# Kernel tuning notes

Hardware: AMD Instinct MI355X
Metric: run time of the kernel (lower is better)

Reference implementation:

```python
import jax, jax.numpy as jnp
import numpy as np

BN_EPS = 1e-5


def setup_inputs() -> dict:
    key = jax.random.key(0)
    ks = jax.random.split(key, 10)
    B, C, L = 16, 512, 1024
    scale = 1.0 / np.sqrt(C)
    inp = {
        "x": jax.random.normal(ks[0], (B, C, L), dtype=jnp.float32),
        "gamma": jnp.ones((C,), jnp.float32),
        "beta": jnp.zeros((C,), jnp.float32),
        "Wq": jax.random.normal(ks[1], (C, C), jnp.float32) * scale,
        "bq": jnp.zeros((C,), jnp.float32),
        "Wk": jax.random.normal(ks[2], (C, C), jnp.float32) * scale,
        "bk": jnp.zeros((C,), jnp.float32),
        "Wv": jax.random.normal(ks[3], (C, C), jnp.float32) * scale,
        "bv": jnp.zeros((C,), jnp.float32),
        "Wp": jax.random.normal(ks[4], (C, C), jnp.float32) * scale,
        "bp": jnp.zeros((C,), jnp.float32),
    }
    return inp


def _pointwise(W, b, h):
    # Conv1d with kernel_size=1 == per-position linear: [C_out,C_in] x [B,C_in,L]
    return jnp.einsum("oc,bcl->bol", W, h) + b[None, :, None]


def reference(x, gamma, beta, Wq, bq, Wk, bk, Wv, bv, Wp, bp):
    B, C, L = x.shape
    # BatchNorm1d (training-mode batch statistics over batch & length dims)
    mean = jnp.mean(x, axis=(0, 2), keepdims=True)
    var = jnp.var(x, axis=(0, 2), keepdims=True)
    hn = (x - mean) * jax.lax.rsqrt(var + BN_EPS)
    hn = hn * gamma[None, :, None] + beta[None, :, None]

    q = _pointwise(Wq, bq, hn)  # [B,C,L]
    k = _pointwise(Wk, bk, hn)
    v = _pointwise(Wv, bv, hn)

    # attn[b,i,j] = sum_c q[b,c,i] k[b,c,j] / sqrt(C); i=query pos, j=key pos
    attn = jnp.einsum("bci,bcj->bij", q, k) * (C ** -0.5)
    attn = jax.nn.softmax(attn, axis=-1)

    # out[b,c,i] = sum_j attn[b,i,j] v[b,c,j]
    h_ = jnp.einsum("bij,bcj->bci", attn, v)
    h_ = _pointwise(Wp, bp, h_)
    return x + h_
```

## Files before the change

### kernel.cpp

```cpp
#include <hip/hip_runtime.h>
#include <hip/hip_bf16.h>


#define BB 16
#define CC 512
#define LL 1024

typedef __bf16 bf16x8 __attribute__((ext_vector_type(8)));
typedef float  f32x4  __attribute__((ext_vector_type(4)));

__device__ inline unsigned short bf16_bits(float f) {
  __hip_bfloat16 h = __float2bfloat16(f);
  return __builtin_bit_cast(unsigned short, h);
}
__device__ inline float bits_lo(unsigned int u) {
  return __builtin_bit_cast(float, u << 16);
}
__device__ inline float bits_hi(unsigned int u) {
  return __builtin_bit_cast(float, u & 0xffff0000u);
}

__global__ __launch_bounds__(256) void bn_stats(
    const float* __restrict__ x, const float* __restrict__ gamma,
    const float* __restrict__ beta, float* __restrict__ scl,
    float* __restrict__ sft, float* __restrict__ rowsum) {
  int c = blockIdx.x;
  int t = threadIdx.x;
  int g = c * 256 + t;
  if (g < 16384) rowsum[g] = 0.f;
  float s = 0.f, s2 = 0.f;
  for (int b = 0; b < BB; ++b) {
    float4 v = ((const float4*)(x + ((size_t)(b * CC + c)) * LL))[t];
    s  += v.x + v.y + v.z + v.w;
    s2 += v.x * v.x + v.y * v.y + v.z * v.z + v.w * v.w;
  }
  for (int m = 32; m; m >>= 1) { s += __shfl_xor(s, m, 64); s2 += __shfl_xor(s2, m, 64); }
  __shared__ float rs[4], rs2[4];
  int wave = t >> 6, lane = t & 63;
  if (lane == 0) { rs[wave] = s; rs2[wave] = s2; }
  __syncthreads();
  if (t == 0) {
    float S  = rs[0] + rs[1] + rs[2] + rs[3];
    float S2 = rs2[0] + rs2[1] + rs2[2] + rs2[3];
    float mean = S * (1.f / 16384.f);
    float var  = S2 * (1.f / 16384.f) - mean * mean;
    float sc = gamma[c] * rsqrtf(var + 1e-5f);
    scl[c] = sc;
    sft[c] = beta[c] - mean * sc;
  }
}

__global__ __launch_bounds__(256) void cast4(
    const float* __restrict__ Wq, const float* __restrict__ Wk,
    const float* __restrict__ Wv, const float* __restrict__ Wp,
    __hip_bfloat16* __restrict__ Wqkv, __hip_bfloat16* __restrict__ Wpb) {
  int m = blockIdx.y;
  const float* src = m == 0 ? Wq : m == 1 ? Wk : m == 2 ? Wv : Wp;
  __hip_bfloat16* dst = m < 3 ? Wqkv + (size_t)m * 262144 : Wpb;
  int i = blockIdx.x * 256 + threadIdx.x;
  float4 v = ((const float4*)src)[i];
  ushort4 o;
  o.x = bf16_bits(v.x); o.y = bf16_bits(v.y);
  o.z = bf16_bits(v.z); o.w = bf16_bits(v.w);
  ((ushort4*)dst)[i] = o;
}

__global__ __launch_bounds__(256) void norm_t(
    const float* __restrict__ x, const float* __restrict__ scl,
    const float* __restrict__ sft, __hip_bfloat16* __restrict__ hnT) {
  __shared__ float tile[32][33];
  int l0 = blockIdx.x * 32, c0 = blockIdx.y * 32, b = blockIdx.z;
  int t = threadIdx.x;
#pragma unroll
  for (int i = 0; i < 4; ++i) {
    int idx = t + i * 256;
    int cc = idx >> 5, ll = idx & 31;
    tile[cc][ll] = x[((size_t)(b * CC + c0 + cc)) * LL + l0 + ll];
  }
  __syncthreads();
#pragma unroll
  for (int i = 0; i < 2; ++i) {
    int idx = t + i * 256;
    int ll = idx >> 4, cc = (idx & 15) * 2;
    float v0 = tile[cc][ll] * scl[c0 + cc] + sft[c0 + cc];
    float v1 = tile[cc + 1][ll] * scl[c0 + cc + 1] + sft[c0 + cc + 1];
    ushort2 o; o.x = bf16_bits(v0); o.y = bf16_bits(v1);
    *(ushort2*)(hnT + ((size_t)(b * LL + l0 + ll)) * CC + c0 + cc) = o;
  }
}

__device__ __forceinline__ void gemm_core(
    const __hip_bfloat16* __restrict__ A, int lda,
    const __hip_bfloat16* __restrict__ B, int ldb, int K,
    __hip_bfloat16* sA, __hip_bfloat16* sB, f32x4 (&acc)[4][4]) {
  const int tid = threadIdx.x;
  const int wave = tid >> 6, lane = tid & 63;
  const int wm = (wave >> 1) * 64, wn = (wave & 1) * 64;
  const int row0 = tid >> 2;
  const int ke0 = (((tid & 3) ^ ((tid >> 3) & 3)) * 8);
  const int fr = lane & 15;
  const int q = lane >> 4;
  const int colA = ((q ^ ((fr >> 1) & 3)) * 8);
  for (int k0 = 0; k0 < K; k0 += 32) {
    __syncthreads();
#pragma unroll
    for (int it = 0; it < 2; ++it) {
      const __hip_bfloat16* ga = A + (size_t)(it * 64 + row0) * lda + (k0 + ke0);
      const __hip_bfloat16* gb = B + (size_t)(it * 64 + row0) * ldb + (k0 + ke0);
      __builtin_amdgcn_global_load_lds(
          (__attribute__((address_space(1))) void*)(void*)ga,
          (__attribute__((address_space(3))) void*)(sA + (it * 256 + wave * 64) * 8),
          16, 0, 0);
      __builtin_amdgcn_global_load_lds(
          (__attribute__((address_space(1))) void*)(void*)gb,
          (__attribute__((address_space(3))) void*)(sB + (it * 256 + wave * 64) * 8),
          16, 0, 0);
    }
    __syncthreads();
    bf16x8 af[4], bfr[4];
#pragma unroll
    for (int i = 0; i < 4; ++i) {
      af[i]  = *(const bf16x8*)(sA + (wm + i * 16 + fr) * 32 + colA);
      bfr[i] = *(const bf16x8*)(sB + (wn + i * 16 + fr) * 32 + colA);
    }
#pragma unroll
    for (int i = 0; i < 4; ++i)
#pragma unroll
      for (int j = 0; j < 4; ++j)
        acc[i][j] = __builtin_amdgcn_mfma_f32_16x16x32_bf16(af[i], bfr[j], acc[i][j], 0, 0, 0);
  }
}

__device__ __forceinline__ void gemm_core8p(
    const __hip_bfloat16* __restrict__ A, int lda,
    const __hip_bfloat16* __restrict__ B, int ldb, int K,
    __hip_bfloat16* sA, __hip_bfloat16* sB, f32x4 (&acc)[8][4]) {
  const int tid = threadIdx.x;
  const int wave = tid >> 6, lane = tid & 63;
  const int fr = lane & 15, q = lane >> 4;
  const int wm = (wave >> 2) * 128, wn = (wave & 3) * 64;
  const int srow = tid >> 3;
  const int sko = ((tid & 7) ^ (srow & 7)) * 8;
  const int NT = K >> 6;
  const int ck0 = (q ^ (fr & 7)) * 8;

#define STG_A(tt, u)                                                           \
  __builtin_amdgcn_global_load_lds(                                            \
      (__attribute__((address_space(1))) void*)(void*)(                        \
          A + (size_t)((u) * 64 + srow) * lda + (tt) * 64 + sko),              \
      (__attribute__((address_space(3))) void*)(                               \
          sA + ((tt) & 1) * 16384 + (u) * 4096 + wave * 512), 16, 0, 0)
#define STG_B(tt, u)                                                           \
  __builtin_amdgcn_global_load_lds(                                            \
      (__attribute__((address_space(1))) void*)(void*)(                        \
          B + (size_t)((u) * 64 + srow) * ldb + (tt) * 64 + sko),              \
      (__attribute__((address_space(3))) void*)(                               \
          sB + ((tt) & 1) * 16384 + (u) * 4096 + wave * 512), 16, 0, 0)

  STG_A(0, 0); STG_A(0, 1); STG_A(0, 2); STG_A(0, 3);
  STG_B(0, 0); STG_B(0, 1); STG_B(0, 2); STG_B(0, 3);
  STG_A(1, 0); STG_A(1, 1); STG_A(1, 2); STG_A(1, 3);
  STG_B(1, 0); STG_B(1, 1); STG_B(1, 2); STG_B(1, 3);

  for (int t = 0; t < NT; ++t) {
    const __hip_bfloat16* pA = sA + (t & 1) * 16384;
    const __hip_bfloat16* pB = sB + (t & 1) * 16384;
    const int rowA = wm + fr, rowB = wn + fr;
    const bool st = (t + 2) < NT;
    bf16x8 a03[4][2], a47[4][2], b01[2][2], b23[2][2];

    __builtin_amdgcn_sched_barrier(0);
    if (t == NT - 1) { asm volatile("s_waitcnt vmcnt(0)" ::: "memory"); }
    else             { asm volatile("s_waitcnt vmcnt(8)" ::: "memory"); }
    __builtin_amdgcn_s_barrier();
    __builtin_amdgcn_sched_barrier(0);

#pragma unroll
    for (int i = 0; i < 4; ++i) {
      a03[i][0] = *(const bf16x8*)(pA + (rowA + i * 16) * 64 + ck0);
      a03[i][1] = *(const bf16x8*)(pA + (rowA + i * 16) * 64 + (ck0 ^ 32));
    }
#pragma unroll
    for (int j = 0; j < 2; ++j) {
      b01[j][0] = *(const bf16x8*)(pB + (rowB + j * 16) * 64 + ck0);
      b01[j][1] = *(const bf16x8*)(pB + (rowB + j * 16) * 64 + (ck0 ^ 32));
    }
    __builtin_amdgcn_s_barrier();
    asm volatile("s_waitcnt lgkmcnt(0)" ::: "memory");
    __builtin_amdgcn_sched_barrier(0);
    __builtin_amdgcn_s_setprio(1);
#pragma unroll
    for (int i = 0; i < 4; ++i)
#pragma unroll
      for (int j = 0; j < 2; ++j) {
        acc[i][j] = __builtin_amdgcn_mfma_f32_16x16x32_bf16(a03[i][0], b01[j][0], acc[i][j], 0, 0, 0);
        acc[i][j] = __builtin_amdgcn_mfma_f32_16x16x32_bf16(a03[i][1], b01[j][1], acc[i][j], 0, 0, 0);
      }
    __builtin_amdgcn_s_setprio(0);
    __builtin_amdgcn_s_barrier();
    __builtin_amdgcn_sched_barrier(0);

#pragma unroll
    for (int j = 0; j < 2; ++j) {
      b23[j][0] = *(const bf16x8*)(pB + (rowB + 32 + j * 16) * 64 + ck0);
      b23[j][1] = *(const bf16x8*)(pB + (rowB + 32 + j * 16) * 64 + (ck0 ^ 32));
    }
    if (st) { STG_A(t + 2, 0); STG_A(t + 2, 2); }
    __builtin_amdgcn_s_barrier();
    asm volatile("s_waitcnt lgkmcnt(0)" ::: "memory");
    __builtin_amdgcn_sched_barrier(0);
    __builtin_amdgcn_s_setprio(1);
#pragma unroll
    for (int i = 0; i < 4; ++i)
#pragma unroll
      for (int j = 0; j < 2; ++j) {
        acc[i][2 + j] = __builtin_amdgcn_mfma_f32_16x16x32_bf16(a03[i][0], b23[j][0], acc[i][2 + j], 0, 0, 0);
        acc[i][2 + j] = __builtin_amdgcn_mfma_f32_16x16x32_bf16(a03[i][1], b23[j][1], acc[i][2 + j], 0, 0, 0);
      }
    __builtin_amdgcn_s_setprio(0);
    __builtin_amdgcn_s_barrier();
    __builtin_amdgcn_sched_barrier(0);

#pragma unroll
    for (int i = 0; i < 4; ++i) {
      a47[i][0] = *(const bf16x8*)(pA + (rowA + 64 + i * 16) * 64 + ck0);
      a47[i][1] = *(const bf16x8*)(pA + (rowA + 64 + i * 16) * 64 + (ck0 ^ 32));
    }
    if (st) { STG_B(t + 2, 0); STG_B(t + 2, 1); STG_B(t + 2, 2); }
    __builtin_amdgcn_s_barrier();
    asm volatile("s_waitcnt lgkmcnt(0)" ::: "memory");
    __builtin_amdgcn_sched_barrier(0);
    __builtin_amdgcn_s_setprio(1);
#pragma unroll
    for (int i = 0; i < 4; ++i)
#pragma unroll
      for (int j = 0; j < 2; ++j) {
        acc[4 + i][j] = __builtin_amdgcn_mfma_f32_16x16x32_bf16(a47[i][0], b01[j][0], acc[4 + i][j], 0, 0, 0);
        acc[4 + i][j] = __builtin_amdgcn_mfma_f32_16x16x32_bf16(a47[i][1], b01[j][1], acc[4 + i][j], 0, 0, 0);
      }
    __builtin_amdgcn_s_setprio(0);
    __builtin_amdgcn_s_barrier();
    __builtin_amdgcn_sched_barrier(0);

    if (st) { STG_B(t + 2, 3); STG_A(t + 2, 1); STG_A(t + 2, 3); }
    __builtin_amdgcn_s_barrier();
    __builtin_amdgcn_sched_barrier(0);
    __builtin_amdgcn_s_setprio(1);
#pragma unroll
    for (int i = 0; i < 4; ++i)
#pragma unroll
      for (int j = 0; j < 2; ++j) {
        acc[4 + i][2 + j] = __builtin_amdgcn_mfma_f32_16x16x32_bf16(a47[i][0], b23[j][0], acc[4 + i][2 + j], 0, 0, 0);
        acc[4 + i][2 + j] = __builtin_amdgcn_mfma_f32_16x16x32_bf16(a47[i][1], b23[j][1], acc[4 + i][2 + j], 0, 0, 0);
      }
    __builtin_amdgcn_s_setprio(0);
  }
#undef STG_A
#undef STG_B
}

__global__ __launch_bounds__(512, 2) void gemm_qkv256(
    const __hip_bfloat16* __restrict__ Wb, const __hip_bfloat16* __restrict__ hnT,
    __hip_bfloat16* __restrict__ qT, __hip_bfloat16* __restrict__ kT,
    __hip_bfloat16* __restrict__ vN,
    const float* __restrict__ bq, const float* __restrict__ bk,
    const float* __restrict__ bv) {
  __shared__ __align__(16) __hip_bfloat16 smem[4 * 16384];
  __hip_bfloat16* sA = smem;
  __hip_bfloat16* sB = smem + 32768;
  const int m0 = blockIdx.y * 256, n0 = blockIdx.x * 256;
  f32x4 acc[8][4] = {};
  gemm_core8p(Wb + (size_t)m0 * 512, 512, hnT + (size_t)n0 * 512, 512, 512,
              sA, sB, acc);
  const int tid = threadIdx.x;
  const int lane = tid & 63, wave = tid >> 6;
  const int wm = (wave >> 2) * 128, wn = (wave & 3) * 64;
  const int crow = (lane >> 4) * 4, ccol = lane & 15;
  const int id = m0 >> 9;
  const int mloc0 = (m0 & 511) + wm;
  const float* bias = id == 0 ? bq : id == 1 ? bk : bv;
  if (id < 2) {
    __hip_bfloat16* D = id == 0 ? qT : kT;
    const int mc0 = m0 & 511;
    __syncthreads();
#pragma unroll
    for (int h = 0; h < 2; ++h) {
      if ((wn >> 7) == h) {
        const int wnL = wn & 127;
#pragma unroll
        for (int i = 0; i < 8; ++i) {
          int mg = mloc0 + i * 16 + crow;
          int mr = wm + i * 16 + crow;
          float bv4[4];
#pragma unroll
          for (int r = 0; r < 4; ++r) bv4[r] = bias[mg + r];
#pragma unroll
          for (int j = 0; j < 4; ++j) {
            int colL = wnL + j * 16 + ccol;
            ushort4 o;
            o.x = bf16_bits(acc[i][j][0] + bv4[0]);
            o.y = bf16_bits(acc[i][j][1] + bv4[1]);
            o.z = bf16_bits(acc[i][j][2] + bv4[2]);
            o.w = bf16_bits(acc[i][j][3] + bv4[3]);
            *(ushort4*)(smem + colL * 264 + mr) = o;
          }
        }
      }
      __syncthreads();
#pragma unroll
      for (int rep = 0; rep < 8; ++rep) {
        int idx = rep * 512 + tid;
        int col = idx >> 5, c8 = idx & 31;
        bf16x8 v = *(const bf16x8*)(smem + col * 264 + c8 * 8);
        *(bf16x8*)(D + (size_t)(n0 + h * 128 + col) * 512 + mc0 + c8 * 8) = v;
      }
      __syncthreads();
    }
  } else {
#pragma unroll
    for (int i = 0; i < 8; ++i) {
      int mg = mloc0 + i * 16 + crow;
      float bv4[4];
#pragma unroll
      for (int r = 0; r < 4; ++r) bv4[r] = bias[mg + r];
#pragma unroll
      for (int j = 0; j < 4; ++j) {
        int ngf = n0 + wn + j * 16 + ccol;
        int b = ngf >> 10, l = ngf & 1023;
        __hip_bfloat16* D = vN + ((size_t)b * CC + mg) * LL + l;
#pragma unroll
        for (int r = 0; r < 4; ++r)
          D[(size_t)r * LL] = __float2bfloat16(acc[i][j][r] + bv4[r]);
      }
    }
  }
}

__global__ __launch_bounds__(512, 2) void gemm_s256_exp(
    const __hip_bfloat16* __restrict__ qT, const __hip_bfloat16* __restrict__ kT,
    __hip_bfloat16* __restrict__ Sb, float* __restrict__ rowsum) {
  __shared__ __align__(16) __hip_bfloat16 sA[2 * 16384];
  __shared__ __align__(16) __hip_bfloat16 sB[2 * 16384];
  const int bat = blockIdx.z;
  const int m0 = blockIdx.y * 256, n0 = blockIdx.x * 256;
  const size_t sLC = (size_t)LL * CC;
  f32x4 acc[8][4] = {};
  gemm_core8p(qT + (size_t)bat * sLC + (size_t)m0 * 512, 512,
              kT + (size_t)bat * sLC + (size_t)n0 * 512, 512, 512,
              sA, sB, acc);
  const int lane = threadIdx.x & 63, wave = threadIdx.x >> 6;
  const int wm = (wave >> 2) * 128, wn = (wave & 3) * 64;
  const int crow = (lane >> 4) * 4, ccol = lane & 15;
  __hip_bfloat16* D = Sb + (size_t)bat * LL * LL;
  float* rs = rowsum + (size_t)bat * LL;
  const float scale = 0.04419417382415922f;
#pragma unroll
  for (int i = 0; i < 8; ++i) {
    int mg = m0 + wm + i * 16 + crow;
    float sp[4] = {0.f, 0.f, 0.f, 0.f};
#pragma unroll
    for (int j = 0; j < 4; ++j) {
      int ng = n0 + wn + j * 16 + ccol;
#pragma unroll
      for (int r = 0; r < 4; ++r) {
        float e = __expf(acc[i][j][r] * scale);
        sp[r] += e;
        D[(size_t)(mg + r) * LL + ng] = __float2bfloat16(e);
      }
    }
#pragma unroll
    for (int r = 0; r < 4; ++r) {
      for (int m = 8; m; m >>= 1) sp[r] += __shfl_xor(sp[r], m, 64);
    }
    if (ccol == 0) {
#pragma unroll
      for (int r = 0; r < 4; ++r) atomicAdd(&rs[mg + r], sp[r]);
    }
  }
}

template <int MODE, bool BIAS>
__global__ __launch_bounds__(256, 3) void gemm_tn(
    const __hip_bfloat16* __restrict__ A, int lda, size_t strideA,
    const __hip_bfloat16* __restrict__ B, int ldb, size_t strideB,
    void* __restrict__ Dp, int ldd, size_t strideD,
    const float* __restrict__ bias, float scale,
    const float* __restrict__ resid, size_t strideR,
    const float* __restrict__ rowdiv, int K) {
  __shared__ __align__(16) __hip_bfloat16 sA[128 * 32];
  __shared__ __align__(16) __hip_bfloat16 sB[128 * 32];
  const int bat = blockIdx.z;
  const int m0 = blockIdx.y * 128, n0 = blockIdx.x * 128;
  f32x4 acc[4][4] = {};
  gemm_core(A + (size_t)bat * strideA + (size_t)m0 * lda, lda,
            B + (size_t)bat * strideB + (size_t)n0 * ldb, ldb, K, sA, sB, acc);
  const int lane = threadIdx.x & 63, wave = threadIdx.x >> 6;
  const int wm = (wave >> 1) * 64, wn = (wave & 1) * 64;
  const int crow = (lane >> 4) * 4, ccol = lane & 15;
  if constexpr (MODE == 0) {
    __hip_bfloat16* D = (__hip_bfloat16*)Dp + (size_t)bat * strideD;
#pragma unroll
    for (int i = 0; i < 4; ++i) {
      int mg = m0 + wm + i * 16 + crow;
      float bv4[4];
#pragma unroll
      for (int r = 0; r < 4; ++r) bv4[r] = BIAS ? bias[mg + r] : 0.f;
#pragma unroll
      for (int j = 0; j < 4; ++j) {
        int ng = n0 + wn + j * 16 + ccol;
#pragma unroll
        for (int r = 0; r < 4; ++r)
          D[(size_t)(mg + r) * ldd + ng] =
              __float2bfloat16(acc[i][j][r] * scale + bv4[r]);
      }
    }
  } else if constexpr (MODE == 1) {
    __hip_bfloat16* D = (__hip_bfloat16*)Dp + (size_t)bat * strideD;
    const float* rsb = rowdiv + (size_t)bat * LL;
#pragma unroll
    for (int i = 0; i < 4; ++i) {
      int mg = m0 + wm + i * 16 + crow;
      float rinv[4];
#pragma unroll
      for (int r = 0; r < 4; ++r) rinv[r] = 1.f / rsb[mg + r];
#pragma unroll
      for (int j = 0; j < 4; ++j) {
        int ng = n0 + wn + j * 16 + ccol;
#pragma unroll
        for (int r = 0; r < 4; ++r)
          D[(size_t)(mg + r) * ldd + ng] =
              __float2bfloat16(acc[i][j][r] * rinv[r]);
      }
    }
  } else {
    float* D = (float*)Dp + (size_t)bat * strideD;
#pragma unroll
    for (int i = 0; i < 4; ++i) {
      int mg = m0 + wm + i * 16 + crow;
      float bv4[4];
#pragma unroll
      for (int r = 0; r < 4; ++r) bv4[r] = BIAS ? bias[mg + r] : 0.f;
#pragma unroll
      for (int j = 0; j < 4; ++j) {
        int ng = n0 + wn + j * 16 + ccol;
        const float* rsrc = resid + (size_t)bat * strideR + (size_t)mg * ldd + ng;
        float* dst = D + (size_t)mg * ldd + ng;
#pragma unroll
        for (int r = 0; r < 4; ++r)
          dst[(size_t)r * ldd] = acc[i][j][r] * scale + bv4[r] + rsrc[(size_t)r * ldd];
      }
    }
  }
}

extern "C" void kernel_launch(void* const* d_in, const int* in_sizes, int n_in,
                              void* d_out, int out_size, void* d_ws, size_t ws_size,
                              hipStream_t stream) {
  const float* x     = (const float*)d_in[0];
  const float* gamma = (const float*)d_in[1];
  const float* beta  = (const float*)d_in[2];
  const float* Wq    = (const float*)d_in[3];
  const float* bq    = (const float*)d_in[4];
  const float* Wk    = (const float*)d_in[5];
  const float* bk    = (const float*)d_in[6];
  const float* Wv    = (const float*)d_in[7];
  const float* bv    = (const float*)d_in[8];
  const float* Wp    = (const float*)d_in[9];
  const float* bp    = (const float*)d_in[10];
  float* out = (float*)d_out;

  char* ws = (char*)d_ws;
  float* scl = (float*)ws;
  float* sft = scl + 512;
  __hip_bfloat16* Wqkvb = (__hip_bfloat16*)(ws + 4096);
  __hip_bfloat16* Wpb = Wqkvb + 786432;
  __hip_bfloat16* hnT = Wpb + 262144;
  __hip_bfloat16* qT  = hnT + 8388608;
  __hip_bfloat16* kT  = qT + 8388608;
  __hip_bfloat16* vN  = kT + 8388608;
  __hip_bfloat16* Sb  = vN + 8388608;
  float* rowsum = (float*)(Sb + 16777216);
  __hip_bfloat16* HT  = hnT;

  bn_stats<<<512, 256, 0, stream>>>(x, gamma, beta, scl, sft, rowsum);
  cast4<<<dim3(256, 4), 256, 0, stream>>>(Wq, Wk, Wv, Wp, Wqkvb, Wpb);
  norm_t<<<dim3(32, 16, 16), 256, 0, stream>>>(x, scl, sft, hnT);

  const size_t sLC = (size_t)LL * CC;
  const size_t sCL = (size_t)CC * LL;
  const size_t sLLb = (size_t)LL * LL;

  gemm_qkv256<<<dim3(64, 6), 512, 0, stream>>>(Wqkvb, hnT, qT, kT, vN, bq, bk, bv);
  gemm_s256_exp<<<dim3(4, 4, 16), 512, 0, stream>>>(qT, kT, Sb, rowsum);
  gemm_tn<1, false><<<dim3(4, 8, 16), 256, 0, stream>>>(
      Sb, 1024, sLLb, vN, 1024, sCL, HT, 512, sLC, nullptr, 1.f, nullptr, 0,
      rowsum, 1024);
  gemm_tn<3, true><<<dim3(8, 4, 16), 256, 0, stream>>>(
      Wpb, 512, 0, HT, 512, sLC, out, 1024, sCL, bp, 1.f, x, sCL, nullptr, 512);
}
```

Baseline: 226.7 us.

## Merge prep kernels, widen norm transpose, stage exp scores through LDS

Folds the BN-stats and weight-cast kernels into one launch, which saves a kernel launch. The normalize-transpose kernel now handles 128-wide tiles, reads x with float4 loads and writes 16-byte bf16 vectors, with scale and shift cached in LDS. The score GEMM epilogue no longer scatters 2-byte exp values to global memory. It stages each half of the tile in padded LDS and then writes coalesced 16-byte rows. This recomputes the exp values and adds several barriers to the epilogue.

```diff
diff --git a/kernel.cpp b/kernel.cpp
--- a/kernel.cpp
+++ b/kernel.cpp
@@ -8,84 +8,93 @@
 
 typedef __bf16 bf16x8 __attribute__((ext_vector_type(8)));
 typedef float  f32x4  __attribute__((ext_vector_type(4)));
+typedef unsigned short u16x8 __attribute__((ext_vector_type(8)));
 
 __device__ inline unsigned short bf16_bits(float f) {
   __hip_bfloat16 h = __float2bfloat16(f);
   return __builtin_bit_cast(unsigned short, h);
 }
-__device__ inline float bits_lo(unsigned int u) {
-  return __builtin_bit_cast(float, u << 16);
-}
-__device__ inline float bits_hi(unsigned int u) {
-  return __builtin_bit_cast(float, u & 0xffff0000u);
-}
-
-__global__ __launch_bounds__(256) void bn_stats(
+
+__global__ __launch_bounds__(256) void prep(
     const float* __restrict__ x, const float* __restrict__ gamma,
     const float* __restrict__ beta, float* __restrict__ scl,
-    float* __restrict__ sft, float* __restrict__ rowsum) {
-  int c = blockIdx.x;
-  int t = threadIdx.x;
-  int g = c * 256 + t;
-  if (g < 16384) rowsum[g] = 0.f;
-  float s = 0.f, s2 = 0.f;
-  for (int b = 0; b < BB; ++b) {
-    float4 v = ((const float4*)(x + ((size_t)(b * CC + c)) * LL))[t];
-    s  += v.x + v.y + v.z + v.w;
-    s2 += v.x * v.x + v.y * v.y + v.z * v.z + v.w * v.w;
-  }
-  for (int m = 32; m; m >>= 1) { s += __shfl_xor(s, m, 64); s2 += __shfl_xor(s2, m, 64); }
-  __shared__ float rs[4], rs2[4];
-  int wave = t >> 6, lane = t & 63;
-  if (lane == 0) { rs[wave] = s; rs2[wave] = s2; }
-  __syncthreads();
-  if (t == 0) {
-    float S  = rs[0] + rs[1] + rs[2] + rs[3];
-    float S2 = rs2[0] + rs2[1] + rs2[2] + rs2[3];
-    float mean = S * (1.f / 16384.f);
-    float var  = S2 * (1.f / 16384.f) - mean * mean;
-    float sc = gamma[c] * rsqrtf(var + 1e-5f);
-    scl[c] = sc;
-    sft[c] = beta[c] - mean * sc;
-  }
-}
-
-__global__ __launch_bounds__(256) void cast4(
+    float* __restrict__ sft, float* __restrict__ rowsum,
     const float* __restrict__ Wq, const float* __restrict__ Wk,
     const float* __restrict__ Wv, const float* __restrict__ Wp,
     __hip_bfloat16* __restrict__ Wqkv, __hip_bfloat16* __restrict__ Wpb) {
-  int m = blockIdx.y;
-  const float* src = m == 0 ? Wq : m == 1 ? Wk : m == 2 ? Wv : Wp;
-  __hip_bfloat16* dst = m < 3 ? Wqkv + (size_t)m * 262144 : Wpb;
-  int i = blockIdx.x * 256 + threadIdx.x;
-  float4 v = ((const float4*)src)[i];
-  ushort4 o;
-  o.x = bf16_bits(v.x); o.y = bf16_bits(v.y);
-  o.z = bf16_bits(v.z); o.w = bf16_bits(v.w);
-  ((ushort4*)dst)[i] = o;
+  __shared__ float rs[4], rs2[4];
+  int bx = blockIdx.x;
+  int t = threadIdx.x;
+  if (bx < 512) {
+    int c = bx;
+    int g = c * 256 + t;
+    if (g < 16384) rowsum[g] = 0.f;
+    float s = 0.f, s2 = 0.f;
+    for (int b = 0; b < BB; ++b) {
+      float4 v = ((const float4*)(x + ((size_t)(b * CC + c)) * LL))[t];
+      s  += v.x + v.y + v.z + v.w;
+      s2 += v.x * v.x + v.y * v.y + v.z * v.z + v.w * v.w;
+    }
+    for (int m = 32; m; m >>= 1) { s += __shfl_xor(s, m, 64); s2 += __shfl_xor(s2, m, 64); }
+    int wave = t >> 6, lane = t & 63;
+    if (lane == 0) { rs[wave] = s; rs2[wave] = s2; }
+    __syncthreads();
+    if (t == 0) {
+      float S  = rs[0] + rs[1] + rs[2] + rs[3];
+      float S2 = rs2[0] + rs2[1] + rs2[2] + rs2[3];
+      float mean = S * (1.f / 16384.f);
+      float var  = S2 * (1.f / 16384.f) - mean * mean;
+      float sc = gamma[c] * rsqrtf(var + 1e-5f);
+      scl[c] = sc;
+      sft[c] = beta[c] - mean * sc;
+    }
+  } else {
+    int cb = bx - 512;
+    int m = cb >> 8;
+    const float* src = m == 0 ? Wq : m == 1 ? Wk : m == 2 ? Wv : Wp;
+    __hip_bfloat16* dst = m < 3 ? Wqkv + (size_t)m * 262144 : Wpb;
+    int i = (cb & 255) * 256 + t;
+    float4 v = ((const float4*)src)[i];
+    ushort4 o;
+    o.x = bf16_bits(v.x); o.y = bf16_bits(v.y);
+    o.z = bf16_bits(v.z); o.w = bf16_bits(v.w);
+    ((ushort4*)dst)[i] = o;
+  }
 }
 
 __global__ __launch_bounds__(256) void norm_t(
     const float* __restrict__ x, const float* __restrict__ scl,
     const float* __restrict__ sft, __hip_bfloat16* __restrict__ hnT) {
-  __shared__ float tile[32][33];
-  int l0 = blockIdx.x * 32, c0 = blockIdx.y * 32, b = blockIdx.z;
+  __shared__ float tile[32][129];
+  __shared__ float s_scl[32], s_sft[32];
+  int l0 = blockIdx.x * 128, c0 = blockIdx.y * 32, b = blockIdx.z;
   int t = threadIdx.x;
-#pragma unroll
-  for (int i = 0; i < 4; ++i) {
-    int idx = t + i * 256;
-    int cc = idx >> 5, ll = idx & 31;
-    tile[cc][ll] = x[((size_t)(b * CC + c0 + cc)) * LL + l0 + ll];
+  if (t < 32) { s_scl[t] = scl[c0 + t]; s_sft[t] = sft[c0 + t]; }
+#pragma unroll
+  for (int it = 0; it < 4; ++it) {
+    int idx = t + it * 256;
+    int cc = idx >> 5, lq = idx & 31;
+    float4 v = *(const float4*)(
+        x + ((size_t)(b * CC + c0 + cc)) * LL + l0 + lq * 4);
+    tile[cc][lq * 4 + 0] = v.x;
+    tile[cc][lq * 4 + 1] = v.y;
+    tile[cc][lq * 4 + 2] = v.z;
+    tile[cc][lq * 4 + 3] = v.w;
   }
   __syncthreads();
 #pragma unroll
-  for (int i = 0; i < 2; ++i) {
-    int idx = t + i * 256;
-    int ll = idx >> 4, cc = (idx & 15) * 2;
-    float v0 = tile[cc][ll] * scl[c0 + cc] + sft[c0 + cc];
-    float v1 = tile[cc + 1][ll] * scl[c0 + cc + 1] + sft[c0 + cc + 1];
-    ushort2 o; o.x = bf16_bits(v0); o.y = bf16_bits(v1);
-    *(ushort2*)(hnT + ((size_t)(b * LL + l0 + ll)) * CC + c0 + cc) = o;
+  for (int it = 0; it < 2; ++it) {
+    int idx = t + it * 256;
+    int ll = idx >> 2;
+    int cq = (idx & 3) * 8;
+    u16x8 o;
+#pragma unroll
+    for (int e = 0; e < 8; ++e) {
+      int c = cq + e;
+      float v = tile[c][ll] * s_scl[c] + s_sft[c];
+      o[e] = bf16_bits(v);
+    }
+    *(u16x8*)(hnT + ((size_t)(b * LL + l0 + ll)) * CC + c0 + cq) = o;
   }
 }
 
@@ -339,8 +348,9 @@
 __global__ __launch_bounds__(512, 2) void gemm_s256_exp(
     const __hip_bfloat16* __restrict__ qT, const __hip_bfloat16* __restrict__ kT,
     __hip_bfloat16* __restrict__ Sb, float* __restrict__ rowsum) {
-  __shared__ __align__(16) __hip_bfloat16 sA[2 * 16384];
-  __shared__ __align__(16) __hip_bfloat16 sB[2 * 16384];
+  __shared__ __align__(16) __hip_bfloat16 smem[4 * 16384];
+  __hip_bfloat16* sA = smem;
+  __hip_bfloat16* sB = smem + 32768;
   const int bat = blockIdx.z;
   const int m0 = blockIdx.y * 256, n0 = blockIdx.x * 256;
   const size_t sLC = (size_t)LL * CC;
@@ -348,7 +358,8 @@
   gemm_core8p(qT + (size_t)bat * sLC + (size_t)m0 * 512, 512,
               kT + (size_t)bat * sLC + (size_t)n0 * 512, 512, 512,
               sA, sB, acc);
-  const int lane = threadIdx.x & 63, wave = threadIdx.x >> 6;
+  const int tid = threadIdx.x;
+  const int lane = tid & 63, wave = tid >> 6;
   const int wm = (wave >> 2) * 128, wn = (wave & 3) * 64;
   const int crow = (lane >> 4) * 4, ccol = lane & 15;
   __hip_bfloat16* D = Sb + (size_t)bat * LL * LL;
@@ -359,15 +370,9 @@
     int mg = m0 + wm + i * 16 + crow;
     float sp[4] = {0.f, 0.f, 0.f, 0.f};
 #pragma unroll
-    for (int j = 0; j < 4; ++j) {
-      int ng = n0 + wn + j * 16 + ccol;
-#pragma unroll
-      for (int r = 0; r < 4; ++r) {
-        float e = __expf(acc[i][j][r] * scale);
-        sp[r] += e;
-        D[(size_t)(mg + r) * LL + ng] = __float2bfloat16(e);
-      }
-    }
+    for (int j = 0; j < 4; ++j)
+#pragma unroll
+      for (int r = 0; r < 4; ++r) sp[r] += __expf(acc[i][j][r] * scale);
 #pragma unroll
     for (int r = 0; r < 4; ++r) {
       for (int m = 8; m; m >>= 1) sp[r] += __shfl_xor(sp[r], m, 64);
@@ -376,6 +381,34 @@
 #pragma unroll
       for (int r = 0; r < 4; ++r) atomicAdd(&rs[mg + r], sp[r]);
     }
+  }
+  unsigned short* s16 = (unsigned short*)smem;
+  __syncthreads();
+#pragma unroll
+  for (int hh = 0; hh < 2; ++hh) {
+    if ((wm >> 7) == hh) {
+      const int mL = wm & 127;
+#pragma unroll
+      for (int i = 0; i < 8; ++i) {
+        int mrow = mL + i * 16 + crow;
+#pragma unroll
+        for (int j = 0; j < 4; ++j) {
+          int ncol = wn + j * 16 + ccol;
+#pragma unroll
+          for (int r = 0; r < 4; ++r)
+            s16[(mrow + r) * 264 + ncol] = bf16_bits(__expf(acc[i][j][r] * scale));
+        }
+      }
+    }
+    __syncthreads();
+#pragma unroll
+    for (int rep = 0; rep < 8; ++rep) {
+      int idx = rep * 512 + tid;
+      int row = idx >> 5, c8 = idx & 31;
+      bf16x8 v = *(const bf16x8*)((const __hip_bfloat16*)smem + row * 264 + c8 * 8);
+      *(bf16x8*)(D + (size_t)(m0 + hh * 128 + row) * LL + n0 + c8 * 8) = v;
+    }
+    __syncthreads();
   }
 }
 
@@ -482,9 +515,9 @@
   float* rowsum = (float*)(Sb + 16777216);
   __hip_bfloat16* HT  = hnT;
 
-  bn_stats<<<512, 256, 0, stream>>>(x, gamma, beta, scl, sft, rowsum);
-  cast4<<<dim3(256, 4), 256, 0, stream>>>(Wq, Wk, Wv, Wp, Wqkvb, Wpb);
-  norm_t<<<dim3(32, 16, 16), 256, 0, stream>>>(x, scl, sft, hnT);
+  prep<<<1536, 256, 0, stream>>>(x, gamma, beta, scl, sft, rowsum,
+                                 Wq, Wk, Wv, Wp, Wqkvb, Wpb);
+  norm_t<<<dim3(8, 16, 16), 256, 0, stream>>>(x, scl, sft, hnT);
 
   const size_t sLC = (size_t)LL * CC;
   const size_t sCL = (size_t)CC * LL;
```

New measurement: 219.9 us. 1.03x faster.
